# Kernel tuning notes

Hardware: AMD Instinct MI355X
Metric: run time of the kernel (lower is better)

The kernel has to match this reference:

```python
import jax, jax.numpy as jnp
import numpy as np
import math

HEADS = 8

def setup_inputs() -> dict:
    key = jax.random.key(0)
    k1, k2 = jax.random.split(key)
    B, C, H, W = 8, 512, 32, 32
    x = jax.random.normal(k1, (B, C, H, W), dtype=jnp.float32)
    # weight-norm 1x1 conv params: v ~ N(0, 0.05), g initialized to ||v|| (torch weight_norm default)
    proj_v = jax.random.normal(k2, (3 * C, C), dtype=jnp.float32) * 0.05
    proj_g = jnp.linalg.norm(proj_v, axis=1)
    proj_b = jnp.zeros((3 * C,), dtype=jnp.float32)
    return {"x": x, "proj_v": proj_v, "proj_g": proj_g, "proj_b": proj_b}

def reference(x, proj_v, proj_g, proj_b):
    B, C, H, W = x.shape
    heads = HEADS
    dim = C // heads
    N = H * W
    # weight-normalized 1x1 conv: w = g * v / ||v|| per output channel
    w = proj_g[:, None] * proj_v / jnp.linalg.norm(proj_v, axis=1, keepdims=True)
    c = jnp.einsum('oc,bchw->bohw', w, x) + proj_b[None, :, None, None]
    c = c.reshape(B, 3, heads, dim, N)
    q, k, v = c[:, 0], c[:, 1], c[:, 2]  # each (B, heads, dim, N)
    scale = 1.0 / math.sqrt(dim)
    attn = jnp.einsum('bhdq,bhdk->bhqk', q, k) * scale  # (B, heads, N, N)
    attn = jax.nn.softmax(attn, axis=-1)
    out = jnp.einsum('bhdk,bhqk->bhdq', v, attn)  # (B, heads, dim, N)
    return x + out.reshape(B, C, H, W)
```

## Files before the change

kernel.cpp:

```cpp
#include <hip/hip_runtime.h>

typedef _Float16 f16;
typedef _Float16 f16x2 __attribute__((ext_vector_type(2)));
typedef _Float16 f16x4 __attribute__((ext_vector_type(4)));
typedef _Float16 f16x8 __attribute__((ext_vector_type(8)));
typedef float f32x4 __attribute__((ext_vector_type(4)));
typedef float f32x16 __attribute__((ext_vector_type(16)));
typedef unsigned int u32;
typedef unsigned int u32x4 __attribute__((ext_vector_type(4)));

__device__ inline f32x16 mfma32(f16x8 a, f16x8 b, f32x16 c) {
    return __builtin_amdgcn_mfma_f32_32x32x16_f16(a, b, c, 0, 0, 0);
}

__device__ inline u32 pk2u(float a, float b) {
    return __builtin_bit_cast(u32, __builtin_amdgcn_cvt_pkrtz(a, b));
}

__global__ __launch_bounds__(256) void prep_k(const float* __restrict__ pv,
                                              const float* __restrict__ pg,
                                              f16* __restrict__ w,
                                              const float* __restrict__ x,
                                              f16* __restrict__ xT) {
    int bid = blockIdx.x;
    if (bid < 1536) {
        int o = bid;
        const float* row = pv + (size_t)o * 512;
        float s = 0.f;
        for (int c = threadIdx.x; c < 512; c += 256) { float t = row[c]; s += t * t; }
        for (int off = 32; off; off >>= 1) s += __shfl_down(s, off, 64);
        __shared__ float red[4];
        int lane = threadIdx.x & 63, wid = threadIdx.x >> 6;
        if (lane == 0) red[wid] = s;
        __syncthreads();
        float tot = red[0] + red[1] + red[2] + red[3];
        float scale = pg[o] * rsqrtf(tot);
        for (int c = threadIdx.x; c < 512; c += 256)
            w[(size_t)o * 512 + c] = (f16)(row[c] * scale);
    } else {
        int t2 = bid - 1536;
        int n0 = (t2 & 31) * 32, c0 = ((t2 >> 5) & 15) * 32, b = t2 >> 9;
        int tx = threadIdx.x & 31, ty = threadIdx.x >> 5;
        __shared__ float t[32][33];
        const float* xb = x + (size_t)b * 512 * 1024;
        for (int i = 0; i < 4; i++)
            t[ty + 8 * i][tx] = xb[(size_t)(c0 + ty + 8 * i) * 1024 + n0 + tx];
        __syncthreads();
        f16* xTb = xT + (size_t)b * 1024 * 512;
        for (int i = 0; i < 4; i++)
            xTb[(size_t)(n0 + ty + 8 * i) * 512 + c0 + tx] = (f16)t[tx][ty + 8 * i];
    }
}

__global__ __launch_bounds__(256) void qkv_gemm_k(const f16* __restrict__ w,
                                                  const f16* __restrict__ xT,
                                                  const float* __restrict__ pb,
                                                  f16* __restrict__ qk,
                                                  f16* __restrict__ v) {
    __shared__ f16 lA[128 * 64];
    __shared__ f16 lB[128 * 64];
    int b = blockIdx.z;
    int oBase = blockIdx.y * 128;
    int nBase = blockIdx.x * 128;
    const f16* xb = xT + (size_t)b * 1024 * 512;
    int tid = threadIdx.x, lane = tid & 63, warp = tid >> 6;
    int wy = warp >> 1, wx = warp & 1;
    int l31 = lane & 31, hi = lane >> 5;

    int srow = lane >> 3;
    int phys = lane & 7;
    int schunk = phys ^ srow;
    const f16* aS[4]; const f16* bS[4]; int ldsOff[4];
    for (int j = 0; j < 4; j++) {
        int rb = (warp * 4 + j) * 8;
        aS[j] = w  + (size_t)(oBase + rb + srow) * 512 + schunk * 8;
        bS[j] = xb + (size_t)(nBase + rb + srow) * 512 + schunk * 8;
        ldsOff[j] = (rb + srow) * 64 + phys * 8;
    }
    int phk[4];
    for (int ks = 0; ks < 4; ks++)
        phk[ks] = (((ks * 2 + hi) ^ (l31 & 7))) * 8;

    f16x8 rA[4], rB[4];
    for (int j = 0; j < 4; j++) {
        rA[j] = *(const f16x8*)aS[j];
        rB[j] = *(const f16x8*)bS[j];
    }

    f32x16 acc[2][2] = {};

    for (int i = 0; i < 8; i++) {
        __syncthreads();
        for (int j = 0; j < 4; j++) {
            *(f16x8*)&lA[ldsOff[j]] = rA[j];
            *(f16x8*)&lB[ldsOff[j]] = rB[j];
        }
        __syncthreads();
        if (i < 7) {
            int k0 = (i + 1) * 64;
            for (int j = 0; j < 4; j++) {
                rA[j] = *(const f16x8*)(aS[j] + k0);
                rB[j] = *(const f16x8*)(bS[j] + k0);
            }
        }
        for (int ks = 0; ks < 4; ks++) {
            f16x8 af[2], bf[2];
            for (int mi = 0; mi < 2; mi++)
                af[mi] = *(f16x8*)&lA[(wy * 64 + mi * 32 + l31) * 64 + phk[ks]];
            for (int ni = 0; ni < 2; ni++)
                bf[ni] = *(f16x8*)&lB[(wx * 64 + ni * 32 + l31) * 64 + phk[ks]];
            for (int mi = 0; mi < 2; mi++)
                for (int ni = 0; ni < 2; ni++)
                    acc[mi][ni] = mfma32(af[mi], bf[ni], acc[mi][ni]);
        }
    }

    int selB = oBase >> 9;
    for (int mi = 0; mi < 2; mi++) {
        for (int g = 0; g < 4; g++) {
            int oR = oBase + wy * 64 + mi * 32 + 8 * g + 4 * hi;
            int h = (oR >> 6) & 7, d0 = oR & 63;
            for (int ni = 0; ni < 2; ni++) {
                int n = nBase + wx * 64 + ni * 32 + l31;
                if (selB < 2) {
                    float sc = selB == 0 ? 0.125f : 1.0f;
                    f16x4 o4;
                    for (int r = 0; r < 4; r++)
                        o4[r] = (f16)((acc[mi][ni][g * 4 + r] + pb[oR + r]) * sc);
                    *(f16x4*)&qk[((((size_t)b * 2 + selB) * 8 + h) * 1024 + n) * 64 + d0] = o4;
                } else {
                    for (int r = 0; r < 4; r++) {
                        float val = acc[mi][ni][g * 4 + r] + pb[oR + r];
                        v[(((size_t)b * 8 + h) * 64 + d0 + r) * 1024 + n] = (f16)val;
                    }
                }
            }
        }
    }
}

#define ATTN_BODY(KT, CUR, NXT)                                                   \
    do {                                                                          \
        f16x8 avC[8];                                                             \
        for (int dt = 0; dt < 2; dt++)                                            \
            for (int ks = 0; ks < 4; ks++)                                        \
                avC[dt * 4 + ks] = *(const f16x8*)&vfrag[(size_t)dt * 32 * 1024   \
                                                         + (KT) * 64 + ks * 16]; \
        if ((KT) < 15)                                                            \
            for (int mt = 0; mt < 2; mt++)                                        \
                for (int ks = 0; ks < 4; ks++)                                    \
                    NXT[mt * 4 + ks] = *(const f16x8*)&kfrag[(size_t)((KT) + 1) * 4096 \
                                                             + mt * 32 * 64 + ks * 16]; \
        u32 P0[2][4], P1[2][4];                                                   \
        float rs = 0.f;                                                           \
        for (int mt = 0; mt < 2; mt++) {                                          \
            f32x16 stt = {};                                                      \
            for (int ks = 0; ks < 4; ks++)                                        \
                stt = mfma32(CUR[mt * 4 + ks], aq[ks], stt);                      \
            for (int g = 0; g < 4; g++) {                                         \
                float p0 = __expf(stt[g * 4 + 0]);                                \
                float p1 = __expf(stt[g * 4 + 1]);                                \
                float p2 = __expf(stt[g * 4 + 2]);                                \
                float p3 = __expf(stt[g * 4 + 3]);                                \
                rs += (p0 + p1) + (p2 + p3);                                      \
                P0[mt][g] = pk2u(p0, p1);                                         \
                P1[mt][g] = pk2u(p2, p3);                                         \
            }                                                                     \
        }                                                                         \
        l_acc += rs;                                                              \
        f16x8 bfrag[4];                                                           \
        for (int ks = 0; ks < 4; ks++) {                                          \
            int mt = ks >> 1, ge = 2 * (ks & 1);                                  \
            u32 e00 = P0[mt][ge], e01 = P0[mt][ge + 1];                           \
            u32 e10 = P1[mt][ge], e11 = P1[mt][ge + 1];                           \
            u32 k0 = hi ? e01 : e00;                                              \
            u32 k1 = hi ? e11 : e10;                                              \
            u32 s0 = hi ? e00 : e01;                                              \
            u32 s1 = hi ? e10 : e11;                                              \
            u32 r0 = __shfl_xor(s0, 32, 64);                                      \
            u32 r1 = __shfl_xor(s1, 32, 64);                                      \
            u32 a0 = hi ? r0 : k0, a1 = hi ? r1 : k1;                             \
            u32 b0 = hi ? k0 : r0, b1 = hi ? k1 : r1;                             \
            u32x4 t = {a0, a1, b0, b1};                                           \
            bfrag[ks] = __builtin_bit_cast(f16x8, t);                             \
        }                                                                         \
        for (int dt = 0; dt < 2; dt++)                                            \
            for (int ks = 0; ks < 4; ks++)                                        \
                accO[dt] = mfma32(avC[dt * 4 + ks], bfrag[ks], accO[dt]);         \
    } while (0)

__global__ __launch_bounds__(256, 2) void attn_k(const f16* __restrict__ qk,
                                                 const f16* __restrict__ vg,
                                                 const float* __restrict__ x,
                                                 float* __restrict__ out) {
    int bh = blockIdx.x;
    int b = bh >> 3, h = bh & 7;
    int qBase = blockIdx.y * 128;
    int tid = threadIdx.x, lane = tid & 63, warp = tid >> 6;
    int l31 = lane & 31, hi = lane >> 5;

    const f16* qbase = qk + (((size_t)b * 2 + 0) * 8 + h) * 1024 * 64;
    const f16* kbase = qk + (((size_t)b * 2 + 1) * 8 + h) * 1024 * 64;
    const f16* vbase = vg + ((size_t)b * 8 + h) * 64 * 1024;

    int q0 = qBase + warp * 32;
    f16x8 aq[4];
    for (int ks = 0; ks < 4; ks++)
        aq[ks] = *(const f16x8*)&qbase[(size_t)(q0 + l31) * 64 + ks * 16 + hi * 8];

    const f16* kfrag = kbase + (size_t)l31 * 64 + hi * 8;
    const f16* vfrag = vbase + (size_t)l31 * 1024 + hi * 8;

    f32x16 accO[2] = {};
    float l_acc = 0.f;

    f16x8 akA[8], akB[8];
    for (int mt = 0; mt < 2; mt++)
        for (int ks = 0; ks < 4; ks++)
            akA[mt * 4 + ks] = *(const f16x8*)&kfrag[(size_t)mt * 32 * 64 + ks * 16];

    for (int kt2 = 0; kt2 < 8; kt2++) {
        ATTN_BODY(kt2 * 2,     akA, akB);
        ATTN_BODY(kt2 * 2 + 1, akB, akA);
    }

    float lt = l_acc + __shfl_xor(l_acc, 32, 64);
    float rl = 1.0f / lt;
    int q = q0 + l31;
    for (int dt = 0; dt < 2; dt++)
        for (int g = 0; g < 4; g++)
            for (int r = 0; r < 4; r++) {
                int d = dt * 32 + 8 * g + 4 * hi + r;
                size_t gi = ((size_t)b * 512 + h * 64 + d) * 1024 + q;
                out[gi] = x[gi] + accO[dt][g * 4 + r] * rl;
            }
}

extern "C" void kernel_launch(void* const* d_in, const int* in_sizes, int n_in,
                              void* d_out, int out_size, void* d_ws, size_t ws_size,
                              hipStream_t stream) {
    (void)in_sizes; (void)n_in; (void)out_size; (void)ws_size;
    const float* x  = (const float*)d_in[0];
    const float* pv = (const float*)d_in[1];
    const float* pg = (const float*)d_in[2];
    const float* pb = (const float*)d_in[3];
    float* out = (float*)d_out;

    char* ws = (char*)d_ws;
    f16* w   = (f16*)(ws);
    f16* xT  = (f16*)(ws + 1572864);
    f16* qk  = (f16*)(ws + 1572864 + 8388608);
    f16* v   = (f16*)(ws + 1572864 + 8388608 + 16777216);

    hipLaunchKernelGGL(prep_k,     dim3(5632),     dim3(256), 0, stream, pv, pg, w, x, xT);
    hipLaunchKernelGGL(qkv_gemm_k, dim3(8, 12, 8), dim3(256), 0, stream, w, xT, pb, qk, v);
    hipLaunchKernelGGL(attn_k,     dim3(64, 8),    dim3(256), 0, stream, qk, v, x, out);
}
```

Baseline: 160.5 us.

## Stage attention K/V tiles through shared memory; use direct global-to-LDS loads in GEMM

The attention kernel now loads 128-key K and V tiles cooperatively into padded, double-buffered shared memory, with a register prefetch staging step. Before, each warp read its K/V fragments directly from global memory. The 128-key tile is split into two halves with separate accumulators, MFMA priority is raised around the PV product, and the grid is transposed so that blocks for the same head run next to each other. The QKV GEMM replaces its register-staged LDS fill with global_load_lds DMA. That GEMM path loses the software prefetch overlap, and the direct loads may not honour the XOR swizzle the old stores applied.

```diff
diff --git a/kernel.cpp b/kernel.cpp
--- a/kernel.cpp
+++ b/kernel.cpp
@@ -15,6 +15,22 @@
 
 __device__ inline u32 pk2u(float a, float b) {
     return __builtin_bit_cast(u32, __builtin_amdgcn_cvt_pkrtz(a, b));
+}
+
+__device__ inline void gl16(const f16* g, f16* l) {
+    __builtin_amdgcn_global_load_lds(
+        (const __attribute__((address_space(1))) void*)g,
+        (__attribute__((address_space(3))) void*)l, 16, 0, 0);
+}
+
+__device__ inline void st8(f16* p, f16x8 v) {
+    *(f16x4*)p = __builtin_shufflevector(v, v, 0, 1, 2, 3);
+    *(f16x4*)(p + 4) = __builtin_shufflevector(v, v, 4, 5, 6, 7);
+}
+__device__ inline f16x8 ld8(const f16* p) {
+    f16x4 lo = *(const f16x4*)p;
+    f16x4 hi = *(const f16x4*)(p + 4);
+    return __builtin_shufflevector(lo, hi, 0, 1, 2, 3, 4, 5, 6, 7);
 }
 
 __global__ __launch_bounds__(256) void prep_k(const float* __restrict__ pv,
@@ -70,39 +86,28 @@
     int srow = lane >> 3;
     int phys = lane & 7;
     int schunk = phys ^ srow;
-    const f16* aS[4]; const f16* bS[4]; int ldsOff[4];
+    const f16* aS[4]; const f16* bS[4]; f16* dA[4]; f16* dB[4];
     for (int j = 0; j < 4; j++) {
         int rb = (warp * 4 + j) * 8;
         aS[j] = w  + (size_t)(oBase + rb + srow) * 512 + schunk * 8;
         bS[j] = xb + (size_t)(nBase + rb + srow) * 512 + schunk * 8;
-        ldsOff[j] = (rb + srow) * 64 + phys * 8;
+        dA[j] = &lA[rb * 64];
+        dB[j] = &lB[rb * 64];
     }
     int phk[4];
     for (int ks = 0; ks < 4; ks++)
         phk[ks] = (((ks * 2 + hi) ^ (l31 & 7))) * 8;
 
-    f16x8 rA[4], rB[4];
-    for (int j = 0; j < 4; j++) {
-        rA[j] = *(const f16x8*)aS[j];
-        rB[j] = *(const f16x8*)bS[j];
-    }
-
     f32x16 acc[2][2] = {};
 
     for (int i = 0; i < 8; i++) {
+        int k0 = i * 64;
         __syncthreads();
         for (int j = 0; j < 4; j++) {
-            *(f16x8*)&lA[ldsOff[j]] = rA[j];
-            *(f16x8*)&lB[ldsOff[j]] = rB[j];
+            gl16(aS[j] + k0, dA[j]);
+            gl16(bS[j] + k0, dB[j]);
         }
         __syncthreads();
-        if (i < 7) {
-            int k0 = (i + 1) * 64;
-            for (int j = 0; j < 4; j++) {
-                rA[j] = *(const f16x8*)(aS[j] + k0);
-                rB[j] = *(const f16x8*)(bS[j] + k0);
-            }
-        }
         for (int ks = 0; ks < 4; ks++) {
             f16x8 af[2], bf[2];
             for (int mi = 0; mi < 2; mi++)
@@ -139,24 +144,40 @@
     }
 }
 
-#define ATTN_BODY(KT, CUR, NXT)                                                   \
+#define ALDK 68
+#define ST (64 * ALDK)
+
+#define LOADT(T)                                                                  \
     do {                                                                          \
-        f16x8 avC[8];                                                             \
-        for (int dt = 0; dt < 2; dt++)                                            \
-            for (int ks = 0; ks < 4; ks++)                                        \
-                avC[dt * 4 + ks] = *(const f16x8*)&vfrag[(size_t)dt * 32 * 1024   \
-                                                         + (KT) * 64 + ks * 16]; \
-        if ((KT) < 15)                                                            \
-            for (int mt = 0; mt < 2; mt++)                                        \
-                for (int ks = 0; ks < 4; ks++)                                    \
-                    NXT[mt * 4 + ks] = *(const f16x8*)&kfrag[(size_t)((KT) + 1) * 4096 \
-                                                             + mt * 32 * 64 + ks * 16]; \
+        for (int j = 0; j < 2; j++) {                                             \
+            int r = sr0 + 32 * j;                                                 \
+            rg[0][j] = *(const f16x8*)&kbase[(size_t)((T) * 128 + r) * 64 + sc0];      \
+            rg[1][j] = *(const f16x8*)&kbase[(size_t)((T) * 128 + 64 + r) * 64 + sc0]; \
+            rg[2][j] = *(const f16x8*)&vbase[(size_t)r * 1024 + (T) * 128 + sc0];      \
+            rg[3][j] = *(const f16x8*)&vbase[(size_t)r * 1024 + (T) * 128 + 64 + sc0]; \
+        }                                                                         \
+    } while (0)
+
+#define STORET(BUF)                                                               \
+    do {                                                                          \
+        for (int t = 0; t < 4; t++)                                               \
+            for (int j = 0; j < 2; j++) {                                         \
+                int r = sr0 + 32 * j;                                             \
+                st8(&smem[((BUF) * 4 + t) * ST + r * ALDK + sc0], rg[t][j]);      \
+            }                                                                     \
+    } while (0)
+
+#define COMPUTE_HALF(KP, VP, ACC)                                                 \
+    do {                                                                          \
         u32 P0[2][4], P1[2][4];                                                   \
         float rs = 0.f;                                                           \
         for (int mt = 0; mt < 2; mt++) {                                          \
+            f16x8 ak[4];                                                          \
+            for (int ks = 0; ks < 4; ks++)                                        \
+                ak[ks] = ld8(&(KP)[(mt * 32 + l31) * ALDK + ks * 16 + hi * 8]);   \
             f32x16 stt = {};                                                      \
             for (int ks = 0; ks < 4; ks++)                                        \
-                stt = mfma32(CUR[mt * 4 + ks], aq[ks], stt);                      \
+                stt = mfma32(ak[ks], aq[ks], stt);                                \
             for (int g = 0; g < 4; g++) {                                         \
                 float p0 = __expf(stt[g * 4 + 0]);                                \
                 float p1 = __expf(stt[g * 4 + 1]);                                \
@@ -168,6 +189,10 @@
             }                                                                     \
         }                                                                         \
         l_acc += rs;                                                              \
+        f16x8 av[2][4];                                                           \
+        for (int dt = 0; dt < 2; dt++)                                            \
+            for (int ks = 0; ks < 4; ks++)                                        \
+                av[dt][ks] = ld8(&(VP)[(dt * 32 + l31) * ALDK + ks * 16 + hi * 8]); \
         f16x8 bfrag[4];                                                           \
         for (int ks = 0; ks < 4; ks++) {                                          \
             int mt = ks >> 1, ge = 2 * (ks & 1);                                  \
@@ -181,21 +206,24 @@
             u32 r1 = __shfl_xor(s1, 32, 64);                                      \
             u32 a0 = hi ? r0 : k0, a1 = hi ? r1 : k1;                             \
             u32 b0 = hi ? k0 : r0, b1 = hi ? k1 : r1;                             \
-            u32x4 t = {a0, a1, b0, b1};                                           \
-            bfrag[ks] = __builtin_bit_cast(f16x8, t);                             \
+            u32x4 tt = {a0, a1, b0, b1};                                          \
+            bfrag[ks] = __builtin_bit_cast(f16x8, tt);                            \
         }                                                                         \
+        __builtin_amdgcn_s_setprio(1);                                            \
         for (int dt = 0; dt < 2; dt++)                                            \
             for (int ks = 0; ks < 4; ks++)                                        \
-                accO[dt] = mfma32(avC[dt * 4 + ks], bfrag[ks], accO[dt]);         \
+                ACC[dt] = mfma32(av[dt][ks], bfrag[ks], ACC[dt]);                 \
+        __builtin_amdgcn_s_setprio(0);                                            \
     } while (0)
 
 __global__ __launch_bounds__(256, 2) void attn_k(const f16* __restrict__ qk,
                                                  const f16* __restrict__ vg,
                                                  const float* __restrict__ x,
                                                  float* __restrict__ out) {
-    int bh = blockIdx.x;
+    __shared__ __align__(16) f16 smem[8 * ST];
+    int bh = blockIdx.y;
     int b = bh >> 3, h = bh & 7;
-    int qBase = blockIdx.y * 128;
+    int qBase = blockIdx.x * 128;
     int tid = threadIdx.x, lane = tid & 63, warp = tid >> 6;
     int l31 = lane & 31, hi = lane >> 5;
 
@@ -208,20 +236,29 @@
     for (int ks = 0; ks < 4; ks++)
         aq[ks] = *(const f16x8*)&qbase[(size_t)(q0 + l31) * 64 + ks * 16 + hi * 8];
 
-    const f16* kfrag = kbase + (size_t)l31 * 64 + hi * 8;
-    const f16* vfrag = vbase + (size_t)l31 * 1024 + hi * 8;
-
-    f32x16 accO[2] = {};
+    int sr0 = tid >> 3, sc0 = (tid & 7) * 8;
+
+    f16x8 rg[4][2];
+    f32x16 accA[2] = {};
+    f32x16 accB[2] = {};
     float l_acc = 0.f;
 
-    f16x8 akA[8], akB[8];
-    for (int mt = 0; mt < 2; mt++)
-        for (int ks = 0; ks < 4; ks++)
-            akA[mt * 4 + ks] = *(const f16x8*)&kfrag[(size_t)mt * 32 * 64 + ks * 16];
-
-    for (int kt2 = 0; kt2 < 8; kt2++) {
-        ATTN_BODY(kt2 * 2,     akA, akB);
-        ATTN_BODY(kt2 * 2 + 1, akB, akA);
+    LOADT(0);
+    STORET(0);
+    LOADT(1);
+    __syncthreads();
+
+    for (int i = 0; i < 8; i++) {
+        int cur = i & 1, nxt = cur ^ 1;
+        if (i < 7) STORET(nxt);
+        if (i < 6) LOADT(i + 2);
+        const f16* K0 = &smem[(cur * 4 + 0) * ST];
+        const f16* K1 = &smem[(cur * 4 + 1) * ST];
+        const f16* V0 = &smem[(cur * 4 + 2) * ST];
+        const f16* V1 = &smem[(cur * 4 + 3) * ST];
+        COMPUTE_HALF(K0, V0, accA);
+        COMPUTE_HALF(K1, V1, accB);
+        __syncthreads();
     }
 
     float lt = l_acc + __shfl_xor(l_acc, 32, 64);
@@ -232,7 +269,7 @@
             for (int r = 0; r < 4; r++) {
                 int d = dt * 32 + 8 * g + 4 * hi + r;
                 size_t gi = ((size_t)b * 512 + h * 64 + d) * 1024 + q;
-                out[gi] = x[gi] + accO[dt][g * 4 + r] * rl;
+                out[gi] = x[gi] + (accA[dt][g * 4 + r] + accB[dt][g * 4 + r]) * rl;
             }
 }
 
@@ -254,5 +291,5 @@
 
     hipLaunchKernelGGL(prep_k,     dim3(5632),     dim3(256), 0, stream, pv, pg, w, x, xT);
     hipLaunchKernelGGL(qkv_gemm_k, dim3(8, 12, 8), dim3(256), 0, stream, w, xT, pb, qk, v);
-    hipLaunchKernelGGL(attn_k,     dim3(64, 8),    dim3(256), 0, stream, qk, v, x, out);
-}
+    hipLaunchKernelGGL(attn_k,     dim3(8, 64),    dim3(256), 0, stream, qk, v, x, out);
+}
```

Result: faster. 139.0 us (-13.4%).
